# Optimization experiments

Measured on AMD Instinct MI355X. Metric: run time of the kernel, lower is better.

Reference implementation:

```python
import jax, jax.numpy as jnp
import numpy as np

M, K, N = 8192, 4096, 12288


def setup_inputs() -> dict:
    key = jax.random.key(0)
    k1, k2, k3, k4 = jax.random.split(key, 4)
    input_tensor = jax.random.normal(k1, (1, M, K), dtype=jnp.float32)
    # int8 quantized weight [N, K] and per-output-channel scale [N, 1]
    weight = jax.random.randint(k2, (N, K), -127, 128, dtype=jnp.int32).astype(jnp.int8)
    weight_scale = (jax.random.uniform(k3, (N, 1), dtype=jnp.float32) * 0.01 + 1e-4)
    bias = jax.random.normal(k4, (N,), dtype=jnp.float32) * 0.1
    return {"input_tensor": input_tensor, "weight": weight,
            "weight_scale": weight_scale, "bias": bias}


def reference(input_tensor, weight, weight_scale, bias):
    x = input_tensor[0]  # squeeze(0) -> [M, K]
    # dynamic per-token symmetric int8 quantization: scale = absmax/127
    a_scale = jnp.max(jnp.abs(x), axis=-1, keepdims=True) / 127.0  # [M, 1]
    q = jnp.clip(jnp.round(x / a_scale), -128.0, 127.0)  # int8 values held in f32
    # int8 GEMM accumulated (emulated in f32), then dequant with per-token x per-channel scales
    acc = jnp.einsum('mk,nk->mn', q, weight.astype(jnp.float32))  # [M, N]
    out = acc * a_scale * weight_scale[:, 0][None, :] + bias[None, :]
    return out[None].astype(input_tensor.dtype)  # unsqueeze(0) -> [1, M, N]
```

## Files before the change

### kernel.cpp

```cpp
#include <hip/hip_runtime.h>
#include <cstdint>

#define M_DIM 8192
#define K_DIM 4096
#define N_DIM 12288
#define KT 64

using i32x4 = __attribute__((ext_vector_type(4))) int;

__device__ inline void gload_lds16(const void* g, void* l) {
    __builtin_amdgcn_global_load_lds(
        (const __attribute__((address_space(1))) void*)g,
        (__attribute__((address_space(3))) void*)l,
        16, 0, 0);
}

__global__ __launch_bounds__(256) void quant_pack(const float* __restrict__ x,
                                                  const int* __restrict__ w32,
                                                  int8_t* __restrict__ qa,
                                                  float* __restrict__ ascale,
                                                  int8_t* __restrict__ wq) {
    const int t = threadIdx.x;
    if (blockIdx.x < M_DIM) {
        const int row = blockIdx.x;
        const float4* xr = (const float4*)(x + (size_t)row * K_DIM);
        float4 v[4];
        float amax = 0.0f;
#pragma unroll
        for (int c = 0; c < 4; ++c) {
            v[c] = xr[t + 256 * c];
            amax = fmaxf(amax, fmaxf(fmaxf(fabsf(v[c].x), fabsf(v[c].y)),
                                     fmaxf(fabsf(v[c].z), fabsf(v[c].w))));
        }
#pragma unroll
        for (int off = 32; off > 0; off >>= 1)
            amax = fmaxf(amax, __shfl_xor(amax, off));
        __shared__ float smax[4];
        if ((t & 63) == 0) smax[t >> 6] = amax;
        __syncthreads();
        amax = fmaxf(fmaxf(smax[0], smax[1]), fmaxf(smax[2], smax[3]));
        const float sc = amax * (1.0f / 127.0f);
        const float inv = (amax > 0.0f) ? (127.0f / amax) : 0.0f;
        if (t == 0) ascale[row] = sc;

        int* q32 = (int*)(qa + (size_t)row * K_DIM);
#pragma unroll
        for (int c = 0; c < 4; ++c) {
            int q0 = (int)rintf(v[c].x * inv);
            int q1 = (int)rintf(v[c].y * inv);
            int q2 = (int)rintf(v[c].z * inv);
            int q3 = (int)rintf(v[c].w * inv);
            q0 = min(127, max(-128, q0));
            q1 = min(127, max(-128, q1));
            q2 = min(127, max(-128, q2));
            q3 = min(127, max(-128, q3));
            q32[t + 256 * c] = (q0 & 255) | ((q1 & 255) << 8) | ((q2 & 255) << 16) | (q3 << 24);
        }
    } else {
        const int pb = blockIdx.x - M_DIM;
        const size_t total4 = (size_t)N_DIM * K_DIM / 4;
        const size_t stride = (size_t)2048 * 256;
        int* out32 = (int*)wq;
        for (size_t i = (size_t)pb * 256 + t; i < total4; i += stride) {
            const int4 v = ((const int4*)w32)[i];
            out32[i] = (v.x & 255) | ((v.y & 255) << 8) | ((v.z & 255) << 16) | (v.w << 24);
        }
    }
}

__global__ __launch_bounds__(512, 2) void gemm_i8(const int8_t* __restrict__ qa,
                                                  const int8_t* __restrict__ wq,
                                                  const float* __restrict__ ascale,
                                                  const float* __restrict__ wscale,
                                                  const float* __restrict__ bias,
                                                  float* __restrict__ out) {
    __shared__ int8_t lds[4][2][16384];

    const int t = threadIdx.x;
    const int lane = t & 63;
    const int wave = t >> 6;
    const int wm = wave >> 2;
    const int wn = wave & 3;
    const int lrow = lane & 15;
    const int lk = lane >> 4;
    const int rslot = (lk ^ ((lrow >> 1) & 3)) << 4;

    const int flat = blockIdx.x;
    const int sw = (flat & 7) * 192 + (flat >> 3);
    const int bm = sw / 48;
    const int bn = sw % 48;

    const int g = (t & 3) ^ ((t >> 3) & 3);
    const size_t aoff0 = (size_t)(bm * 256 + (t >> 2)) * K_DIM + (size_t)g * 16;
    const size_t aoff1 = aoff0 + (size_t)128 * K_DIM;
    const size_t boff0 = (size_t)(bn * 256 + (t >> 2)) * K_DIM + (size_t)g * 16;
    const size_t boff1 = boff0 + (size_t)128 * K_DIM;

#define STAGE_ALL(sb, jt)                                                     \
    {                                                                         \
        gload_lds16(qa + aoff0 + (size_t)(jt) * 64, &lds[sb][0][t * 16]);     \
        gload_lds16(qa + aoff1 + (size_t)(jt) * 64, &lds[sb][0][t * 16 + 8192]); \
        gload_lds16(wq + boff0 + (size_t)(jt) * 64, &lds[sb][1][t * 16]);     \
        gload_lds16(wq + boff1 + (size_t)(jt) * 64, &lds[sb][1][t * 16 + 8192]); \
    }

    i32x4 acc[8][4] = {};
    i32x4 fa0[8], fb0[4], fa1[8], fb1[4];

#pragma unroll
    for (int p = 0; p < 3; ++p) STAGE_ALL(p, p);
    asm volatile("s_waitcnt vmcnt(8)" ::: "memory");
    __builtin_amdgcn_s_barrier();
    __builtin_amdgcn_sched_barrier(0);
    {
        const int8_t* __restrict__ LA = lds[0][0];
        const int8_t* __restrict__ LB = lds[0][1];
#pragma unroll
        for (int nf = 0; nf < 4; ++nf)
            fb0[nf] = *(const i32x4*)&LB[(wn * 64 + nf * 16 + lrow) * 64 + rslot];
#pragma unroll
        for (int mf = 0; mf < 8; ++mf)
            fa0[mf] = *(const i32x4*)&LA[(wm * 128 + mf * 16 + lrow) * 64 + rslot];
    }

#define ITER(J, CA, CB, NA, NB)                                               \
    do {                                                                      \
        if ((J) + 3 < KT) {                                                   \
            STAGE_ALL(((J) + 3) & 3, (J) + 3);                                \
            asm volatile("s_waitcnt vmcnt(8)" ::: "memory");                  \
        } else if ((J) + 2 < KT) {                                            \
            asm volatile("s_waitcnt vmcnt(4)" ::: "memory");                  \
        } else if ((J) + 1 < KT) {                                            \
            asm volatile("s_waitcnt vmcnt(0)" ::: "memory");                  \
        }                                                                     \
        __builtin_amdgcn_s_barrier();                                         \
        __builtin_amdgcn_sched_barrier(0);                                    \
        if ((J) + 1 < KT) {                                                   \
            const int8_t* __restrict__ LA = lds[((J) + 1) & 3][0];            \
            const int8_t* __restrict__ LB = lds[((J) + 1) & 3][1];            \
            _Pragma("unroll")                                                 \
            for (int nf = 0; nf < 4; ++nf)                                    \
                NB[nf] = *(const i32x4*)&LB[(wn * 64 + nf * 16 + lrow) * 64 + rslot]; \
            _Pragma("unroll")                                                 \
            for (int mf = 0; mf < 8; ++mf)                                    \
                NA[mf] = *(const i32x4*)&LA[(wm * 128 + mf * 16 + lrow) * 64 + rslot]; \
        }                                                                     \
        __builtin_amdgcn_sched_barrier(0);                                    \
        __builtin_amdgcn_s_setprio(1);                                        \
        _Pragma("unroll")                                                     \
        for (int mf = 0; mf < 8; ++mf)                                        \
            _Pragma("unroll")                                                 \
            for (int nf = 0; nf < 4; ++nf)                                    \
                acc[mf][nf] = __builtin_amdgcn_mfma_i32_16x16x64_i8(          \
                    CA[mf], CB[nf], acc[mf][nf], 0, 0, 0);                    \
        __builtin_amdgcn_s_setprio(0);                                        \
        asm volatile("s_waitcnt lgkmcnt(0)" ::: "memory");                    \
        __builtin_amdgcn_sched_barrier(0);                                    \
    } while (0)

    for (int j = 0; j < KT; j += 2) {
        ITER(j, fa0, fb0, fa1, fb1);
        ITER(j + 1, fa1, fb1, fa0, fb0);
    }

    const int r0 = bm * 256 + wm * 128;
    const int c0 = bn * 256 + wn * 64;
    float asc[8][4];
#pragma unroll
    for (int m = 0; m < 8; ++m)
#pragma unroll
        for (int jj = 0; jj < 4; ++jj)
            asc[m][jj] = ascale[r0 + m * 16 + lk * 4 + jj];
#pragma unroll
    for (int n = 0; n < 4; ++n) {
        const int col = c0 + n * 16 + lrow;
        const float wsc = wscale[col];
        const float bb = bias[col];
#pragma unroll
        for (int m = 0; m < 8; ++m) {
#pragma unroll
            for (int jj = 0; jj < 4; ++jj) {
                const int row = r0 + m * 16 + lk * 4 + jj;
                out[(size_t)row * N_DIM + col] = (float)acc[m][n][jj] * asc[m][jj] * wsc + bb;
            }
        }
    }
}

extern "C" void kernel_launch(void* const* d_in, const int* in_sizes, int n_in,
                              void* d_out, int out_size, void* d_ws, size_t ws_size,
                              hipStream_t stream) {
    const float* x = (const float*)d_in[0];
    const int* w32 = (const int*)d_in[1];
    const float* wscale = (const float*)d_in[2];
    const float* bias = (const float*)d_in[3];
    float* out = (float*)d_out;

    int8_t* qa = (int8_t*)d_ws;
    float* ascale = (float*)((char*)d_ws + (size_t)M_DIM * K_DIM);
    int8_t* wq = (int8_t*)((char*)d_ws + (size_t)M_DIM * K_DIM +
                           (size_t)M_DIM * sizeof(float));

    quant_pack<<<M_DIM + 2048, 256, 0, stream>>>(x, w32, qa, ascale, wq);
    gemm_i8<<<1536, 512, 0, stream>>>(qa, wq, ascale, wscale, bias, out);
}
```

Baseline: 543.2 us.

## Split K-iteration into two half-phases interleaving LDS reads, staging and MFMA

Restructures the int8 GEMM main loop into two phases per K-tile: each computes half the M fragments while the other half's LDS reads and separate A/B global-to-LDS staging are in flight. Prefetch depth drops from three tiles ahead to two, and an extra barrier is added per tile. The aim is finer-grained overlap of LDS reads, global loads and MFMA work, with fewer live fragment registers. The cost is more barriers and a shallower global prefetch.

```diff
diff --git a/kernel.cpp b/kernel.cpp
--- a/kernel.cpp
+++ b/kernel.cpp
@@ -96,71 +96,119 @@
     const size_t boff0 = (size_t)(bn * 256 + (t >> 2)) * K_DIM + (size_t)g * 16;
     const size_t boff1 = boff0 + (size_t)128 * K_DIM;
 
-#define STAGE_ALL(sb, jt)                                                     \
-    {                                                                         \
-        gload_lds16(qa + aoff0 + (size_t)(jt) * 64, &lds[sb][0][t * 16]);     \
+#define STAGE_A(sb, jt)                                                        \
+    {                                                                          \
+        gload_lds16(qa + aoff0 + (size_t)(jt) * 64, &lds[sb][0][t * 16]);      \
         gload_lds16(qa + aoff1 + (size_t)(jt) * 64, &lds[sb][0][t * 16 + 8192]); \
-        gload_lds16(wq + boff0 + (size_t)(jt) * 64, &lds[sb][1][t * 16]);     \
+    }
+#define STAGE_B(sb, jt)                                                        \
+    {                                                                          \
+        gload_lds16(wq + boff0 + (size_t)(jt) * 64, &lds[sb][1][t * 16]);      \
         gload_lds16(wq + boff1 + (size_t)(jt) * 64, &lds[sb][1][t * 16 + 8192]); \
     }
 
+#define READ_AHI(s)                                                            \
+    {                                                                          \
+        _Pragma("unroll") for (int mf = 0; mf < 4; ++mf)                       \
+            ahi[mf] = *(const i32x4*)&lds[s][0][(wm * 128 + (mf + 4) * 16 +    \
+                                                lrow) * 64 + rslot];           \
+    }
+#define READ_NEXT(s, ALO, BN)                                                  \
+    {                                                                          \
+        _Pragma("unroll") for (int nf = 0; nf < 4; ++nf)                       \
+            BN[nf] = *(const i32x4*)&lds[s][1][(wn * 64 + nf * 16 + lrow) * 64 + rslot]; \
+        _Pragma("unroll") for (int mf = 0; mf < 4; ++mf)                       \
+            ALO[mf] = *(const i32x4*)&lds[s][0][(wm * 128 + mf * 16 + lrow) * 64 + rslot]; \
+    }
+#define MMLO(ALO, BC)                                                          \
+    {                                                                          \
+        __builtin_amdgcn_s_setprio(1);                                         \
+        _Pragma("unroll") for (int mf = 0; mf < 4; ++mf)                       \
+            _Pragma("unroll") for (int nf = 0; nf < 4; ++nf)                   \
+                acc[mf][nf] = __builtin_amdgcn_mfma_i32_16x16x64_i8(           \
+                    ALO[mf], BC[nf], acc[mf][nf], 0, 0, 0);                    \
+        __builtin_amdgcn_s_setprio(0);                                         \
+    }
+#define MMHI(BC)                                                               \
+    {                                                                          \
+        __builtin_amdgcn_s_setprio(1);                                         \
+        _Pragma("unroll") for (int mf = 0; mf < 4; ++mf)                       \
+            _Pragma("unroll") for (int nf = 0; nf < 4; ++nf)                   \
+                acc[mf + 4][nf] = __builtin_amdgcn_mfma_i32_16x16x64_i8(       \
+                    ahi[mf], BC[nf], acc[mf + 4][nf], 0, 0, 0);                \
+        __builtin_amdgcn_s_setprio(0);                                         \
+    }
+#define SB0 __builtin_amdgcn_sched_barrier(0);
+#define BAR __builtin_amdgcn_s_barrier();
+#define WAIT_LGKM(n) asm volatile("s_waitcnt lgkmcnt(" #n ")" ::: "memory");
+#define WAIT_VM(n) asm volatile("s_waitcnt vmcnt(" #n ")" ::: "memory");
+
+#define PH0(J, ALO, BC)                                                        \
+    {                                                                          \
+        READ_AHI((J) & 3);                                                     \
+        STAGE_A(((J) + 2) & 3, (J) + 2);                                       \
+        WAIT_VM(2);                                                            \
+        SB0;                                                                   \
+        BAR;                                                                   \
+        WAIT_LGKM(4);                                                          \
+        SB0;                                                                   \
+        MMLO(ALO, BC);                                                         \
+    }
+#define PH1(J, BC, ALON, BN)                                                   \
+    {                                                                          \
+        READ_NEXT(((J) + 1) & 3, ALON, BN);                                    \
+        STAGE_B(((J) + 2) & 3, (J) + 2);                                       \
+        SB0;                                                                   \
+        BAR;                                                                   \
+        WAIT_LGKM(8);                                                          \
+        SB0;                                                                   \
+        MMHI(BC);                                                              \
+    }
+
     i32x4 acc[8][4] = {};
-    i32x4 fa0[8], fb0[4], fa1[8], fb1[4];
-
-#pragma unroll
-    for (int p = 0; p < 3; ++p) STAGE_ALL(p, p);
-    asm volatile("s_waitcnt vmcnt(8)" ::: "memory");
-    __builtin_amdgcn_s_barrier();
-    __builtin_amdgcn_sched_barrier(0);
+    i32x4 alo0[4], b0[4], alo1[4], b1[4], ahi[4];
+
+    STAGE_A(0, 0);
+    STAGE_B(0, 0);
+    STAGE_A(1, 1);
+    STAGE_B(1, 1);
+    WAIT_VM(4);
+    SB0;
+    BAR;
+    READ_NEXT(0, alo0, b0);
+
+    for (int jp = 0; jp < 31; ++jp) {
+        const int j = jp * 2;
+        PH0(j, alo0, b0);
+        PH1(j, b0, alo1, b1);
+        PH0(j + 1, alo1, b1);
+        PH1(j + 1, b1, alo0, b0);
+    }
+
     {
-        const int8_t* __restrict__ LA = lds[0][0];
-        const int8_t* __restrict__ LB = lds[0][1];
-#pragma unroll
-        for (int nf = 0; nf < 4; ++nf)
-            fb0[nf] = *(const i32x4*)&LB[(wn * 64 + nf * 16 + lrow) * 64 + rslot];
-#pragma unroll
-        for (int mf = 0; mf < 8; ++mf)
-            fa0[mf] = *(const i32x4*)&LA[(wm * 128 + mf * 16 + lrow) * 64 + rslot];
-    }
-
-#define ITER(J, CA, CB, NA, NB)                                               \
-    do {                                                                      \
-        if ((J) + 3 < KT) {                                                   \
-            STAGE_ALL(((J) + 3) & 3, (J) + 3);                                \
-            asm volatile("s_waitcnt vmcnt(8)" ::: "memory");                  \
-        } else if ((J) + 2 < KT) {                                            \
-            asm volatile("s_waitcnt vmcnt(4)" ::: "memory");                  \
-        } else if ((J) + 1 < KT) {                                            \
-            asm volatile("s_waitcnt vmcnt(0)" ::: "memory");                  \
-        }                                                                     \
-        __builtin_amdgcn_s_barrier();                                         \
-        __builtin_amdgcn_sched_barrier(0);                                    \
-        if ((J) + 1 < KT) {                                                   \
-            const int8_t* __restrict__ LA = lds[((J) + 1) & 3][0];            \
-            const int8_t* __restrict__ LB = lds[((J) + 1) & 3][1];            \
-            _Pragma("unroll")                                                 \
-            for (int nf = 0; nf < 4; ++nf)                                    \
-                NB[nf] = *(const i32x4*)&LB[(wn * 64 + nf * 16 + lrow) * 64 + rslot]; \
-            _Pragma("unroll")                                                 \
-            for (int mf = 0; mf < 8; ++mf)                                    \
-                NA[mf] = *(const i32x4*)&LA[(wm * 128 + mf * 16 + lrow) * 64 + rslot]; \
-        }                                                                     \
-        __builtin_amdgcn_sched_barrier(0);                                    \
-        __builtin_amdgcn_s_setprio(1);                                        \
-        _Pragma("unroll")                                                     \
-        for (int mf = 0; mf < 8; ++mf)                                        \
-            _Pragma("unroll")                                                 \
-            for (int nf = 0; nf < 4; ++nf)                                    \
-                acc[mf][nf] = __builtin_amdgcn_mfma_i32_16x16x64_i8(          \
-                    CA[mf], CB[nf], acc[mf][nf], 0, 0, 0);                    \
-        __builtin_amdgcn_s_setprio(0);                                        \
-        asm volatile("s_waitcnt lgkmcnt(0)" ::: "memory");                    \
-        __builtin_amdgcn_sched_barrier(0);                                    \
-    } while (0)
-
-    for (int j = 0; j < KT; j += 2) {
-        ITER(j, fa0, fb0, fa1, fb1);
-        ITER(j + 1, fa1, fb1, fa0, fb0);
+        READ_AHI(62 & 3);
+        WAIT_VM(0);
+        SB0;
+        BAR;
+        WAIT_LGKM(4);
+        SB0;
+        MMLO(alo0, b0);
+
+        READ_NEXT(63 & 3, alo1, b1);
+        SB0;
+        BAR;
+        WAIT_LGKM(8);
+        SB0;
+        MMHI(b0);
+    }
+    {
+        READ_AHI(63 & 3);
+        WAIT_LGKM(4);
+        SB0;
+        MMLO(alo1, b1);
+        WAIT_LGKM(0);
+        SB0;
+        MMHI(b1);
     }
 
     const int r0 = bm * 256 + wm * 128;
```

Measured after the change: 537.7 us. No clear change (-1.0%).
